# Kernel optimization log

Hardware: AMD Instinct MI355X
Metric: run time of the kernel (lower is better)

The kernel has to match this reference:

```python
import jax, jax.numpy as jnp
import numpy as np

DIM = 1024
N_HEADS = 16
HEAD_DIM = DIM // N_HEADS
SCALE = HEAD_DIM ** 0.5


def setup_inputs() -> dict:
    key = jax.random.key(0)
    k_x, k_wqkv, k_bqkv, k_wp, k_bp = jax.random.split(key, 5)
    B, S = 4, 2048
    x = jax.random.normal(k_x, (B, S, DIM), dtype=jnp.float32)
    # Linear params stored input-major: y = x @ W + b
    std_qkv = 1.0 / np.sqrt(DIM)
    W_qkv = jax.random.uniform(k_wqkv, (DIM, 3 * DIM), jnp.float32, -std_qkv, std_qkv)
    b_qkv = jax.random.uniform(k_bqkv, (3 * DIM,), jnp.float32, -std_qkv, std_qkv)
    W_proj = jax.random.uniform(k_wp, (DIM, DIM), jnp.float32, -std_qkv, std_qkv)
    b_proj = jax.random.uniform(k_bp, (DIM,), jnp.float32, -std_qkv, std_qkv)
    return {"x": x, "W_qkv": W_qkv, "b_qkv": b_qkv, "W_proj": W_proj, "b_proj": b_proj}


def reference(x, W_qkv, b_qkv, W_proj, b_proj):
    B, S, D = x.shape
    qkv = x @ W_qkv + b_qkv                       # [B,S,3D]
    Q, K, V = jnp.split(qkv, 3, axis=-1)          # each [B,S,D]
    def heads(t):                                 # [B,S,D] -> [B,H,S,hd]
        return t.reshape(B, S, N_HEADS, HEAD_DIM).transpose(0, 2, 1, 3)
    Q, K, V = heads(Q), heads(K), heads(V)
    scores = jnp.einsum('bhqd,bhkd->bhqk', Q, K) / SCALE   # [B,H,S,S]
    attn = jax.nn.softmax(scores, axis=-1)
    out = jnp.einsum('bhqk,bhkd->bhqd', attn, V)           # [B,H,S,hd]
    out = out.transpose(0, 2, 1, 3).reshape(B, S, D)
    return out @ W_proj + b_proj
```

## Files before the change

kernel.cpp:

```cpp
#include <hip/hip_runtime.h>
#include <hip/hip_bf16.h>

typedef __attribute__((ext_vector_type(8))) __bf16 bf16x8;
typedef __attribute__((ext_vector_type(4))) float f32x4;
typedef __attribute__((ext_vector_type(16))) float f32x16;
typedef __attribute__((ext_vector_type(4))) unsigned int u32x4;

#define DIM 1024
#define NHEADS 16
#define HDIM 64
#define BATCH 4
#define SEQ 2048
#define ROWS (BATCH * SEQ)
#define SCL 0.18033688011112042f

__device__ inline unsigned short f2bf(float f) {
    __hip_bfloat16 h = __float2bfloat16(f);
    return *reinterpret_cast<unsigned short*>(&h);
}

__device__ inline unsigned int packbf2(float a, float b) {
    unsigned short ua = __builtin_bit_cast(unsigned short, (__bf16)a);
    unsigned short ub = __builtin_bit_cast(unsigned short, (__bf16)b);
    return (unsigned int)ua | ((unsigned int)ub << 16);
}

typedef const __attribute__((address_space(1))) unsigned int* gas_ptr;
typedef __attribute__((address_space(3))) unsigned int* las_ptr;
__device__ inline void gload16(const void* g, void* l) {
    __builtin_amdgcn_global_load_lds((gas_ptr)g, (las_ptr)l, 16, 0, 0);
}

__global__ __launch_bounds__(256) void cast_f32_bf16(const float* __restrict__ in,
                                                     unsigned short* __restrict__ out,
                                                     int n4) {
    int i = blockIdx.x * 256 + threadIdx.x;
    if (i < n4) {
        float4 v = ((const float4*)in)[i];
        ushort4 o;
        o.x = f2bf(v.x); o.y = f2bf(v.y); o.z = f2bf(v.z); o.w = f2bf(v.w);
        ((ushort4*)out)[i] = o;
    }
}

__global__ __launch_bounds__(256) void transpose_cast(const float* __restrict__ in,
                                                      unsigned short* __restrict__ out,
                                                      int R, int C, int srows, float scl) {
    __shared__ float tile[32][33];
    int c0 = blockIdx.x * 32, r0 = blockIdx.y * 32;
    int tx = threadIdx.x & 31, ty = threadIdx.x >> 5;
#pragma unroll
    for (int i = 0; i < 32; i += 8) {
        int r = r0 + ty + i, c = c0 + tx;
        tile[ty + i][tx] = in[(size_t)r * C + c];
    }
    __syncthreads();
#pragma unroll
    for (int i = 0; i < 32; i += 8) {
        int orow = c0 + ty + i, oc = r0 + tx;
        float v = tile[tx][ty + i];
        if (orow < srows) v *= scl;
        out[(size_t)orow * R + oc] = f2bf(v);
    }
}

__global__ __launch_bounds__(256) void gemm_bt_bias(const unsigned short* __restrict__ A,
                                                    const unsigned short* __restrict__ Bt,
                                                    const float* __restrict__ bias,
                                                    unsigned short* __restrict__ Cq,
                                                    unsigned short* __restrict__ Kp,
                                                    unsigned short* __restrict__ Vp,
                                                    float* __restrict__ Cf,
                                                    int M, int N, int K, int qcols) {
    __shared__ unsigned short SMEM[18432];
    unsigned short* As0 = SMEM;
    unsigned short* Bs0 = SMEM + 8192;
    const int tid = threadIdx.x;
    const int lane = tid & 63, wave = tid >> 6;
    const int wm = (wave >> 1) * 64, wn = (wave & 1) * 64;
    const int nwg = gridDim.x * gridDim.y;
    const int gflat = blockIdx.y * gridDim.x + blockIdx.x;
    const int bidx = (gflat & 7) * (nwg >> 3) + (gflat >> 3);
    const int bx = bidx % gridDim.x, byy = bidx / gridDim.x;
    const int rowA = byy * 128, rowB = bx * 128;
    const int fr = lane & 15, fo = (lane >> 4) * 8;

    f32x4 acc[4][4] = {};

    for (int k0 = 0; k0 < K; k0 += 64) {
#pragma unroll
        for (int kc = 0; kc < 2; kc++) {
#pragma unroll
            for (int c = 0; c < 2; c++) {
                int o = c * 4096 + tid * 16;
                int r = o >> 6, cb = o & 63;
                int ldsb = c * 4096 + wave * 1024;
                gload16((const char*)A + ((size_t)(rowA + r) * K + k0 + kc * 32) * 2 + cb,
                        (char*)As0 + kc * 8192 + ldsb);
                gload16((const char*)Bt + ((size_t)(rowB + r) * K + k0 + kc * 32) * 2 + cb,
                        (char*)Bs0 + kc * 8192 + ldsb);
            }
        }
        __syncthreads();
#pragma unroll
        for (int kc = 0; kc < 2; kc++) {
            bf16x8 af[4], bfr[4];
#pragma unroll
            for (int i = 0; i < 4; i++) {
                af[i]  = *(const bf16x8*)(As0 + kc * 4096 + (wm + i * 16 + fr) * 32 + fo);
                bfr[i] = *(const bf16x8*)(Bs0 + kc * 4096 + (wn + i * 16 + fr) * 32 + fo);
            }
#pragma unroll
            for (int mi = 0; mi < 4; mi++)
#pragma unroll
                for (int ni = 0; ni < 4; ni++)
                    acc[mi][ni] = __builtin_amdgcn_mfma_f32_16x16x32_bf16(af[mi], bfr[ni],
                                                                          acc[mi][ni], 0, 0, 0);
        }
        __syncthreads();
    }

    const int cn = lane & 15, cm = (lane >> 4) * 4;
    const int gn0 = rowB + wn;

    if (Cf) {
        for (int ni = 0; ni < 4; ni++) {
            int gn = gn0 + ni * 16 + cn;
            float bv = bias[gn];
            if (gn < qcols) bv *= SCL;
            for (int mi = 0; mi < 4; mi++) {
#pragma unroll
                for (int r = 0; r < 4; r++) {
                    int gm = rowA + wm + mi * 16 + cm + r;
                    Cf[(size_t)gm * N + gn] = acc[mi][ni][r] + bv;
                }
            }
        }
    } else if (gn0 < 1024) {
        for (int ni = 0; ni < 4; ni++) {
            int gn = gn0 + ni * 16 + cn;
            float bv = bias[gn];
            if (gn < qcols) bv *= SCL;
            for (int mi = 0; mi < 4; mi++) {
#pragma unroll
                for (int r = 0; r < 4; r++) {
                    int gm = rowA + wm + mi * 16 + cm + r;
                    Cq[(size_t)gm * 1024 + gn] = f2bf(acc[mi][ni][r] + bv);
                }
            }
        }
    } else {
        unsigned short* Lw = SMEM + wave * (64 * 72);
        for (int ni = 0; ni < 4; ni++) {
            float bv = bias[gn0 + ni * 16 + cn];
            for (int mi = 0; mi < 4; mi++) {
#pragma unroll
                for (int r = 0; r < 4; r++)
                    Lw[(mi * 16 + cm + r) * 72 + ni * 16 + cn] = f2bf(acc[mi][ni][r] + bv);
            }
        }
        __builtin_amdgcn_s_waitcnt(0);
        const int b = rowA >> 11, s0g = rowA & 2047;
        const int mm = lane & 31, hh = lane >> 5;
        if (gn0 < 2048) {
            const int h = (gn0 - 1024) >> 6;
            const size_t by = (size_t)(b * 16 + h);
            const int kub = (s0g + wm) >> 5;
#pragma unroll
            for (int f = 0; f < 8; f++) {
                int ktl = f >> 2, ks = f & 3;
                uint4 d = *(const uint4*)&Lw[(ktl * 32 + mm) * 72 + ks * 16 + hh * 8];
                *(uint4*)(Kp + ((by * 64 + kub + ktl) * 4 + ks) * 512 + lane * 8) = d;
            }
        } else {
            const int h = (gn0 - 2048) >> 6;
            const size_t by = (size_t)(b * 16 + h);
            const int vub = (s0g + wm) >> 4;
#pragma unroll
            for (int f = 0; f < 8; f++) {
                int ksl = f >> 1, dt = f & 1;
                unsigned short tmp[8];
#pragma unroll
                for (int j = 0; j < 8; j++)
                    tmp[j] = Lw[(ksl * 16 + (j & 3) + 8 * (j >> 2) + 4 * hh) * 72 + dt * 32 + mm];
                *(uint4*)(Vp + ((by * 128 + vub + ksl) * 2 + dt) * 512 + lane * 8) =
                    *(uint4*)tmp;
            }
        }
    }
}

__device__ inline void softmax_pv(const f32x16& cfrag, const bf16x8 vf[2][2],
                                  f32x16& o0, f32x16& o1, float& psum) {
    unsigned int pk[8];
    float es[8];
#pragma unroll
    for (int p = 0; p < 8; p++) {
        float e0 = __builtin_amdgcn_exp2f(cfrag[2 * p]);
        float e1 = __builtin_amdgcn_exp2f(cfrag[2 * p + 1]);
        es[p] = e0 + e1;
        pk[p] = packbf2(e0, e1);
    }
    psum += ((es[0] + es[1]) + (es[2] + es[3])) + ((es[4] + es[5]) + (es[6] + es[7]));
    u32x4 lo = {pk[0], pk[1], pk[2], pk[3]};
    u32x4 hi = {pk[4], pk[5], pk[6], pk[7]};
    bf16x8 pa0 = __builtin_bit_cast(bf16x8, lo);
    bf16x8 pa1 = __builtin_bit_cast(bf16x8, hi);
    o0 = __builtin_amdgcn_mfma_f32_32x32x16_bf16(pa0, vf[0][0], o0, 0, 0, 0);
    o1 = __builtin_amdgcn_mfma_f32_32x32x16_bf16(pa0, vf[0][1], o1, 0, 0, 0);
    o0 = __builtin_amdgcn_mfma_f32_32x32x16_bf16(pa1, vf[1][0], o0, 0, 0, 0);
    o1 = __builtin_amdgcn_mfma_f32_32x32x16_bf16(pa1, vf[1][1], o1, 0, 0, 0);
}

__device__ inline void attn_step(const bf16x8 kf[4], const bf16x8 vf[2][2],
                                 const bf16x8 qf[2][4], f32x16 oacc[2][2], float psum[2]) {
    f32x16 cf0 = {}, cf1 = {};
#pragma unroll
    for (int ks = 0; ks < 4; ks++)
        cf0 = __builtin_amdgcn_mfma_f32_32x32x16_bf16(kf[ks], qf[0][ks], cf0, 0, 0, 0);
#pragma unroll
    for (int ks = 0; ks < 4; ks++)
        cf1 = __builtin_amdgcn_mfma_f32_32x32x16_bf16(kf[ks], qf[1][ks], cf1, 0, 0, 0);
    softmax_pv(cf0, vf, oacc[0][0], oacc[0][1], psum[0]);
    softmax_pv(cf1, vf, oacc[1][0], oacc[1][1], psum[1]);
}

__global__ __launch_bounds__(256, 2) void attn_kernel(const unsigned short* __restrict__ Qb,
                                                      const unsigned short* __restrict__ Kp,
                                                      const unsigned short* __restrict__ Vp,
                                                      unsigned short* __restrict__ attnb) {
    __shared__ float Po[2][8 * 256];
    __shared__ float Pl[2][128];
    const int tid = threadIdx.x;
    const int lane = tid & 63, wave = tid >> 6;
    const int qpair = wave >> 1, ksplit = wave & 1;
    const int m31 = lane & 31, h = lane >> 5;
    const int gflat = blockIdx.y * gridDim.x + blockIdx.x;
    const int xcd = gflat & 7, slot = gflat >> 3;
    const int by = xcd * 8 + (slot >> 4);
    const int qb = slot & 15;
    const int b = by >> 4;
    const int bS = b * SEQ, hcol = (by & 15) * HDIM;
    const int q0 = qb * 128 + qpair * 64;

    bf16x8 qf[2][4];
#pragma unroll
    for (int qt = 0; qt < 2; qt++)
#pragma unroll
        for (int ks = 0; ks < 4; ks++)
            qf[qt][ks] = *(const bf16x8*)(Qb + (size_t)(bS + q0 + qt * 32 + m31) * 1024 +
                                          hcol + ks * 16 + h * 8);

    f32x16 oacc[2][2] = {};
    float psum[2] = {0.f, 0.f};

    const unsigned short* kbase = Kp + (size_t)by * 64 * 2048 + lane * 8;
    const unsigned short* vbase = Vp + (size_t)by * 128 * 1024 + lane * 8;

    const int ku0 = ksplit * 32;
    bf16x8 kfa[4], kfb[4];
    {
        const unsigned short* kp = kbase + (size_t)ku0 * 2048;
#pragma unroll
        for (int ks = 0; ks < 4; ks++) kfa[ks] = *(const bf16x8*)(kp + ks * 512);
    }
    for (int ki = 0; ki < 32; ki += 2) {
        {
            int ku = ku0 + ki;
            bf16x8 vf[2][2];
#pragma unroll
            for (int ks = 0; ks < 2; ks++) {
                const unsigned short* vp = vbase + ((size_t)ku * 2 + ks) * 1024;
                vf[ks][0] = *(const bf16x8*)(vp);
                vf[ks][1] = *(const bf16x8*)(vp + 512);
            }
            const unsigned short* kpn = kbase + (size_t)(ku + 1) * 2048;
#pragma unroll
            for (int ks = 0; ks < 4; ks++) kfb[ks] = *(const bf16x8*)(kpn + ks * 512);
            attn_step(kfa, vf, qf, oacc, psum);
        }
        {
            int ku = ku0 + ki + 1;
            bf16x8 vf[2][2];
#pragma unroll
            for (int ks = 0; ks < 2; ks++) {
                const unsigned short* vp = vbase + ((size_t)ku * 2 + ks) * 1024;
                vf[ks][0] = *(const bf16x8*)(vp);
                vf[ks][1] = *(const bf16x8*)(vp + 512);
            }
            int kup = ku0 + ((ki + 2 < 32) ? (ki + 2) : 31);
            const unsigned short* kpn = kbase + (size_t)kup * 2048;
#pragma unroll
            for (int ks = 0; ks < 4; ks++) kfa[ks] = *(const bf16x8*)(kpn + ks * 512);
            attn_step(kfb, vf, qf, oacc, psum);
        }
    }

#pragma unroll
    for (int qt = 0; qt < 2; qt++) {
        if (ksplit == 1) {
#pragma unroll
            for (int dt = 0; dt < 2; dt++)
#pragma unroll
                for (int c = 0; c < 4; c++) {
                    f32x4 v = {oacc[qt][dt][c * 4 + 0], oacc[qt][dt][c * 4 + 1],
                               oacc[qt][dt][c * 4 + 2], oacc[qt][dt][c * 4 + 3]};
                    *(f32x4*)&Po[qpair][(dt * 4 + c) * 256 + lane * 4] = v;
                }
            if (qt == 0)
                *(float2*)&Pl[qpair][lane * 2] = make_float2(psum[0], psum[1]);
        }
        __syncthreads();
        if (ksplit == 0) {
#pragma unroll
            for (int dt = 0; dt < 2; dt++)
#pragma unroll
                for (int c = 0; c < 4; c++) {
                    f32x4 v = *(const f32x4*)&Po[qpair][(dt * 4 + c) * 256 + lane * 4];
#pragma unroll
                    for (int j = 0; j < 4; j++) oacc[qt][dt][c * 4 + j] += v[j];
                }
            if (qt == 0) {
                float2 pl = *(const float2*)&Pl[qpair][lane * 2];
                psum[0] += pl.x; psum[1] += pl.y;
            }
        }
        if (qt == 0) __syncthreads();
    }

    if (ksplit == 0) {
#pragma unroll
        for (int qt = 0; qt < 2; qt++) {
            float lt = psum[qt] + __shfl_xor(psum[qt], 32, 64);
            float rl = 1.f / lt;
#pragma unroll
            for (int r = 0; r < 16; r++) {
                int row = (r & 3) + 8 * (r >> 2) + 4 * h;
                float rlr = __shfl(rl, row, 64);
                size_t orow = (size_t)(bS + q0 + qt * 32 + row) * 1024 + hcol;
                attnb[orow + m31]      = f2bf(oacc[qt][0][r] * rlr);
                attnb[orow + 32 + m31] = f2bf(oacc[qt][1][r] * rlr);
            }
        }
    }
}

extern "C" void kernel_launch(void* const* d_in, const int* in_sizes, int n_in,
                              void* d_out, int out_size, void* d_ws, size_t ws_size,
                              hipStream_t stream) {
    const float* x      = (const float*)d_in[0];
    const float* W_qkv  = (const float*)d_in[1];
    const float* b_qkv  = (const float*)d_in[2];
    const float* W_proj = (const float*)d_in[3];
    const float* b_proj = (const float*)d_in[4];
    float* out = (float*)d_out;

    char* ws = (char*)d_ws;
    unsigned short* x_bf   = (unsigned short*)(ws);
    unsigned short* WqkvT  = (unsigned short*)(ws + 16777216);
    unsigned short* Qb     = (unsigned short*)(ws + 23068672);
    unsigned short* Kp     = (unsigned short*)(ws + 39845888);
    unsigned short* Vp     = (unsigned short*)(ws + 56623104);
    unsigned short* WprojT = (unsigned short*)(ws + 73400320);
    unsigned short* attnb  = (unsigned short*)(ws);

    cast_f32_bf16<<<(ROWS * DIM / 4 + 255) / 256, 256, 0, stream>>>(x, x_bf, ROWS * DIM / 4);
    transpose_cast<<<dim3(3 * DIM / 32, DIM / 32), 256, 0, stream>>>(W_qkv, WqkvT, DIM, 3 * DIM, DIM, SCL);
    transpose_cast<<<dim3(DIM / 32, DIM / 32), 256, 0, stream>>>(W_proj, WprojT, DIM, DIM, 0, 1.f);

    gemm_bt_bias<<<dim3(3 * DIM / 128, ROWS / 128), 256, 0, stream>>>(
        x_bf, WqkvT, b_qkv, Qb, Kp, Vp, nullptr, ROWS, 3 * DIM, DIM, DIM);

    attn_kernel<<<dim3(SEQ / 128, BATCH * NHEADS), 256, 0, stream>>>(Qb, Kp, Vp, attnb);

    gemm_bt_bias<<<dim3(DIM / 128, ROWS / 128), 256, 0, stream>>>(
        attnb, WprojT, b_proj, nullptr, nullptr, nullptr, out, ROWS, DIM, DIM, 0);
}
```

Baseline: 271.8 us.

## Halve attention query tile per block and fuse prologue cast/transpose kernels

```diff
diff --git a/kernel.cpp b/kernel.cpp
--- a/kernel.cpp
+++ b/kernel.cpp
@@ -31,23 +31,34 @@
     __builtin_amdgcn_global_load_lds((gas_ptr)g, (las_ptr)l, 16, 0, 0);
 }
 
-__global__ __launch_bounds__(256) void cast_f32_bf16(const float* __restrict__ in,
-                                                     unsigned short* __restrict__ out,
-                                                     int n4) {
-    int i = blockIdx.x * 256 + threadIdx.x;
-    if (i < n4) {
-        float4 v = ((const float4*)in)[i];
+__global__ __launch_bounds__(256) void prologue(const float* __restrict__ x,
+                                                unsigned short* __restrict__ x_bf,
+                                                const float* __restrict__ W_qkv,
+                                                unsigned short* __restrict__ WqkvT,
+                                                const float* __restrict__ W_proj,
+                                                unsigned short* __restrict__ WprojT) {
+    __shared__ float tile[32][33];
+    const int blk = blockIdx.x;
+    if (blk < 8192) {
+        int i = blk * 256 + threadIdx.x;
+        float4 v = ((const float4*)x)[i];
         ushort4 o;
         o.x = f2bf(v.x); o.y = f2bf(v.y); o.z = f2bf(v.z); o.w = f2bf(v.w);
-        ((ushort4*)out)[i] = o;
-    }
-}
-
-__global__ __launch_bounds__(256) void transpose_cast(const float* __restrict__ in,
-                                                      unsigned short* __restrict__ out,
-                                                      int R, int C, int srows, float scl) {
-    __shared__ float tile[32][33];
-    int c0 = blockIdx.x * 32, r0 = blockIdx.y * 32;
+        ((ushort4*)x_bf)[i] = o;
+        return;
+    }
+    const float* in; unsigned short* outp; int C, srows, bx, byy; float scl;
+    if (blk < 11264) {
+        int t = blk - 8192;
+        in = W_qkv; outp = WqkvT; C = 3 * DIM; srows = DIM; scl = SCL;
+        bx = t % 96; byy = t / 96;
+    } else {
+        int t = blk - 11264;
+        in = W_proj; outp = WprojT; C = DIM; srows = 0; scl = 1.f;
+        bx = t & 31; byy = t >> 5;
+    }
+    const int R = DIM;
+    int c0 = bx * 32, r0 = byy * 32;
     int tx = threadIdx.x & 31, ty = threadIdx.x >> 5;
 #pragma unroll
     for (int i = 0; i < 32; i += 8) {
@@ -60,7 +71,7 @@
         int orow = c0 + ty + i, oc = r0 + tx;
         float v = tile[tx][ty + i];
         if (orow < srows) v *= scl;
-        out[(size_t)orow * R + oc] = f2bf(v);
+        outp[(size_t)orow * R + oc] = f2bf(v);
     }
 }
 
@@ -212,47 +223,32 @@
     o1 = __builtin_amdgcn_mfma_f32_32x32x16_bf16(pa1, vf[1][1], o1, 0, 0, 0);
 }
 
-__device__ inline void attn_step(const bf16x8 kf[4], const bf16x8 vf[2][2],
-                                 const bf16x8 qf[2][4], f32x16 oacc[2][2], float psum[2]) {
-    f32x16 cf0 = {}, cf1 = {};
-#pragma unroll
-    for (int ks = 0; ks < 4; ks++)
-        cf0 = __builtin_amdgcn_mfma_f32_32x32x16_bf16(kf[ks], qf[0][ks], cf0, 0, 0, 0);
-#pragma unroll
-    for (int ks = 0; ks < 4; ks++)
-        cf1 = __builtin_amdgcn_mfma_f32_32x32x16_bf16(kf[ks], qf[1][ks], cf1, 0, 0, 0);
-    softmax_pv(cf0, vf, oacc[0][0], oacc[0][1], psum[0]);
-    softmax_pv(cf1, vf, oacc[1][0], oacc[1][1], psum[1]);
-}
-
 __global__ __launch_bounds__(256, 2) void attn_kernel(const unsigned short* __restrict__ Qb,
                                                       const unsigned short* __restrict__ Kp,
                                                       const unsigned short* __restrict__ Vp,
                                                       unsigned short* __restrict__ attnb) {
     __shared__ float Po[2][8 * 256];
-    __shared__ float Pl[2][128];
+    __shared__ float Pl[2][64];
     const int tid = threadIdx.x;
     const int lane = tid & 63, wave = tid >> 6;
-    const int qpair = wave >> 1, ksplit = wave & 1;
+    const int qh = wave >> 1, ksplit = wave & 1;
     const int m31 = lane & 31, h = lane >> 5;
     const int gflat = blockIdx.y * gridDim.x + blockIdx.x;
     const int xcd = gflat & 7, slot = gflat >> 3;
-    const int by = xcd * 8 + (slot >> 4);
-    const int qb = slot & 15;
+    const int by = xcd * 8 + (slot >> 5);
+    const int qb = slot & 31;
     const int b = by >> 4;
     const int bS = b * SEQ, hcol = (by & 15) * HDIM;
-    const int q0 = qb * 128 + qpair * 64;
-
-    bf16x8 qf[2][4];
-#pragma unroll
-    for (int qt = 0; qt < 2; qt++)
-#pragma unroll
-        for (int ks = 0; ks < 4; ks++)
-            qf[qt][ks] = *(const bf16x8*)(Qb + (size_t)(bS + q0 + qt * 32 + m31) * 1024 +
-                                          hcol + ks * 16 + h * 8);
-
-    f32x16 oacc[2][2] = {};
-    float psum[2] = {0.f, 0.f};
+    const int q0 = qb * 64 + qh * 32;
+
+    bf16x8 qf[4];
+#pragma unroll
+    for (int ks = 0; ks < 4; ks++)
+        qf[ks] = *(const bf16x8*)(Qb + (size_t)(bS + q0 + m31) * 1024 +
+                                  hcol + ks * 16 + h * 8);
+
+    f32x16 oacc[2] = {};
+    float psum = 0.f;
 
     const unsigned short* kbase = Kp + (size_t)by * 64 * 2048 + lane * 8;
     const unsigned short* vbase = Vp + (size_t)by * 128 * 1024 + lane * 8;
@@ -277,7 +273,11 @@
             const unsigned short* kpn = kbase + (size_t)(ku + 1) * 2048;
 #pragma unroll
             for (int ks = 0; ks < 4; ks++) kfb[ks] = *(const bf16x8*)(kpn + ks * 512);
-            attn_step(kfa, vf, qf, oacc, psum);
+            f32x16 cf = {};
+#pragma unroll
+            for (int ks = 0; ks < 4; ks++)
+                cf = __builtin_amdgcn_mfma_f32_32x32x16_bf16(kfa[ks], qf[ks], cf, 0, 0, 0);
+            softmax_pv(cf, vf, oacc[0], oacc[1], psum);
         }
         {
             int ku = ku0 + ki + 1;
@@ -292,55 +292,46 @@
             const unsigned short* kpn = kbase + (size_t)kup * 2048;
 #pragma unroll
             for (int ks = 0; ks < 4; ks++) kfa[ks] = *(const bf16x8*)(kpn + ks * 512);
-            attn_step(kfb, vf, qf, oacc, psum);
-        }
-    }
-
-#pragma unroll
-    for (int qt = 0; qt < 2; qt++) {
-        if (ksplit == 1) {
-#pragma unroll
-            for (int dt = 0; dt < 2; dt++)
-#pragma unroll
-                for (int c = 0; c < 4; c++) {
-                    f32x4 v = {oacc[qt][dt][c * 4 + 0], oacc[qt][dt][c * 4 + 1],
-                               oacc[qt][dt][c * 4 + 2], oacc[qt][dt][c * 4 + 3]};
-                    *(f32x4*)&Po[qpair][(dt * 4 + c) * 256 + lane * 4] = v;
-                }
-            if (qt == 0)
-                *(float2*)&Pl[qpair][lane * 2] = make_float2(psum[0], psum[1]);
-        }
-        __syncthreads();
-        if (ksplit == 0) {
-#pragma unroll
-            for (int dt = 0; dt < 2; dt++)
-#pragma unroll
-                for (int c = 0; c < 4; c++) {
-                    f32x4 v = *(const f32x4*)&Po[qpair][(dt * 4 + c) * 256 + lane * 4];
-#pragma unroll
-                    for (int j = 0; j < 4; j++) oacc[qt][dt][c * 4 + j] += v[j];
-                }
-            if (qt == 0) {
-                float2 pl = *(const float2*)&Pl[qpair][lane * 2];
-                psum[0] += pl.x; psum[1] += pl.y;
-            }
-        }
-        if (qt == 0) __syncthreads();
-    }
-
+            f32x16 cf = {};
+#pragma unroll
+            for (int ks = 0; ks < 4; ks++)
+                cf = __builtin_amdgcn_mfma_f32_32x32x16_bf16(kfb[ks], qf[ks], cf, 0, 0, 0);
+            softmax_pv(cf, vf, oacc[0], oacc[1], psum);
+        }
+    }
+
+    if (ksplit == 1) {
+#pragma unroll
+        for (int dt = 0; dt < 2; dt++)
+#pragma unroll
+            for (int c = 0; c < 4; c++) {
+                f32x4 v = {oacc[dt][c * 4 + 0], oacc[dt][c * 4 + 1],
+                           oacc[dt][c * 4 + 2], oacc[dt][c * 4 + 3]};
+                *(f32x4*)&Po[qh][(dt * 4 + c) * 256 + lane * 4] = v;
+            }
+        Pl[qh][lane] = psum;
+    }
+    __syncthreads();
     if (ksplit == 0) {
 #pragma unroll
-        for (int qt = 0; qt < 2; qt++) {
-            float lt = psum[qt] + __shfl_xor(psum[qt], 32, 64);
-            float rl = 1.f / lt;
-#pragma unroll
-            for (int r = 0; r < 16; r++) {
-                int row = (r & 3) + 8 * (r >> 2) + 4 * h;
-                float rlr = __shfl(rl, row, 64);
-                size_t orow = (size_t)(bS + q0 + qt * 32 + row) * 1024 + hcol;
-                attnb[orow + m31]      = f2bf(oacc[qt][0][r] * rlr);
-                attnb[orow + 32 + m31] = f2bf(oacc[qt][1][r] * rlr);
-            }
+        for (int dt = 0; dt < 2; dt++)
+#pragma unroll
+            for (int c = 0; c < 4; c++) {
+                f32x4 v = *(const f32x4*)&Po[qh][(dt * 4 + c) * 256 + lane * 4];
+#pragma unroll
+                for (int j = 0; j < 4; j++) oacc[dt][c * 4 + j] += v[j];
+            }
+        psum += Pl[qh][lane];
+
+        float lt = psum + __shfl_xor(psum, 32, 64);
+        float rl = 1.f / lt;
+#pragma unroll
+        for (int r = 0; r < 16; r++) {
+            int row = (r & 3) + 8 * (r >> 2) + 4 * h;
+            float rlr = __shfl(rl, row, 64);
+            size_t orow = (size_t)(bS + q0 + row) * 1024 + hcol;
+            attnb[orow + m31]      = f2bf(oacc[0][r] * rlr);
+            attnb[orow + 32 + m31] = f2bf(oacc[1][r] * rlr);
         }
     }
 }
@@ -364,14 +355,12 @@
     unsigned short* WprojT = (unsigned short*)(ws + 73400320);
     unsigned short* attnb  = (unsigned short*)(ws);
 
-    cast_f32_bf16<<<(ROWS * DIM / 4 + 255) / 256, 256, 0, stream>>>(x, x_bf, ROWS * DIM / 4);
-    transpose_cast<<<dim3(3 * DIM / 32, DIM / 32), 256, 0, stream>>>(W_qkv, WqkvT, DIM, 3 * DIM, DIM, SCL);
-    transpose_cast<<<dim3(DIM / 32, DIM / 32), 256, 0, stream>>>(W_proj, WprojT, DIM, DIM, 0, 1.f);
+    prologue<<<12288, 256, 0, stream>>>(x, x_bf, W_qkv, WqkvT, W_proj, WprojT);
 
     gemm_bt_bias<<<dim3(3 * DIM / 128, ROWS / 128), 256, 0, stream>>>(
         x_bf, WqkvT, b_qkv, Qb, Kp, Vp, nullptr, ROWS, 3 * DIM, DIM, DIM);
 
-    attn_kernel<<<dim3(SEQ / 128, BATCH * NHEADS), 256, 0, stream>>>(Qb, Kp, Vp, attnb);
+    attn_kernel<<<dim3(SEQ / 64, BATCH * NHEADS), 256, 0, stream>>>(Qb, Kp, Vp, attnb);
 
     gemm_bt_bias<<<dim3(DIM / 128, ROWS / 128), 256, 0, stream>>>(
         attnb, WprojT, b_proj, nullptr, nullptr, nullptr, out, ROWS, DIM, DIM, 0);
```

After: 329.7 us. +21.3%, slower.
